# Performance work log

Hardware: AMD Instinct MI355X
Metric: run time of the kernel (lower is better)

## Reference

```python
import jax, jax.numpy as jnp
import numpy as np

K = 8
B = 3.0
DIM = 32
HID = 32
BATCH = 65536
MIN_BW = 1e-3
MIN_BH = 1e-3
MIN_D = 1e-3


def setup_inputs() -> dict:
    key = jax.random.key(0)
    ks = jax.random.split(key, 8)
    L = DIM - 1
    x = jax.random.normal(ks[0], (BATCH, DIM), jnp.float32)
    init_param = jax.random.uniform(ks[1], (3 * K - 1,), jnp.float32, -0.5, 0.5)
    # stacked per-dim FCNN weights; layer l conditions on x[:, :l+1] -> causal zero-mask
    w1 = jax.random.normal(ks[2], (L, L, HID), jnp.float32) * 0.2
    mask = (jnp.arange(L)[None, :] <= jnp.arange(L)[:, None]).astype(jnp.float32)
    w1 = w1 * mask[:, :, None]
    b1 = jax.random.normal(ks[3], (L, HID), jnp.float32) * 0.1
    w2 = jax.random.normal(ks[4], (L, HID, HID), jnp.float32) * 0.2
    b2 = jax.random.normal(ks[5], (L, HID), jnp.float32) * 0.1
    w3 = jax.random.normal(ks[6], (L, HID, 3 * K - 1), jnp.float32) * 0.2
    b3 = jax.random.normal(ks[7], (L, 3 * K - 1), jnp.float32) * 0.1
    return {"x": x, "init_param": init_param, "w1": w1, "b1": b1,
            "w2": w2, "b2": b2, "w3": w3, "b3": b3}


def _rqs_forward(x, Wu, Hu, Du):
    # x: [dim, batch]; Wu, Hu: [dim, batch, K]; Du: [dim, batch, K-1]
    inside = (x >= -B) & (x <= B)
    xc = jnp.clip(x, -B, B)
    # bin widths
    widths = jax.nn.softmax(Wu, axis=-1)
    widths = MIN_BW + (1.0 - MIN_BW * K) * widths
    cw = jnp.cumsum(widths, axis=-1)
    cw = jnp.concatenate([jnp.zeros(cw.shape[:-1] + (1,), cw.dtype), cw], axis=-1)
    cw = 2.0 * B * cw - B
    cw = cw.at[..., 0].set(-B).at[..., -1].set(B)
    widths = cw[..., 1:] - cw[..., :-1]
    # bin heights
    heights = jax.nn.softmax(Hu, axis=-1)
    heights = MIN_BH + (1.0 - MIN_BH * K) * heights
    ch = jnp.cumsum(heights, axis=-1)
    ch = jnp.concatenate([jnp.zeros(ch.shape[:-1] + (1,), ch.dtype), ch], axis=-1)
    ch = 2.0 * B * ch - B
    ch = ch.at[..., 0].set(-B).at[..., -1].set(B)
    heights = ch[..., 1:] - ch[..., :-1]
    # knot derivatives, edges pinned so softplus(const)+min_d = 1
    const = float(np.log(np.exp(1.0 - MIN_D) - 1.0))
    pad = jnp.full(Du.shape[:-1] + (1,), const, Du.dtype)
    derivs = MIN_D + jax.nn.softplus(jnp.concatenate([pad, Du, pad], axis=-1))  # [.., K+1]
    # bin search (searchsorted on cumwidths, eps bump on last edge)
    cw_s = cw.at[..., -1].add(1e-6)
    idx = jnp.sum((xc[..., None] >= cw_s).astype(jnp.int32), axis=-1) - 1
    idx = jnp.clip(idx, 0, K - 1)
    g = lambda a: jnp.take_along_axis(a, idx[..., None], axis=-1)[..., 0]
    in_cw = g(cw)
    in_w = g(widths)
    in_ch = g(ch)
    in_h = g(heights)
    in_delta = g(heights / widths)
    d0 = g(derivs)
    d1 = g(derivs[..., 1:])
    theta = (xc - in_cw) / in_w
    tt = theta * (1.0 - theta)
    num = in_h * (in_delta * theta ** 2 + d0 * tt)
    den = in_delta + (d0 + d1 - 2.0 * in_delta) * tt
    out = in_ch + num / den
    dnum = in_delta ** 2 * (d1 * theta ** 2 + 2.0 * in_delta * tt + d0 * (1.0 - theta) ** 2)
    ld = jnp.log(dnum) - 2.0 * jnp.log(den)
    out = jnp.where(inside, out, x)  # identity tails
    ld = jnp.where(inside, ld, 0.0)
    return out, ld


def reference(x, init_param, w1, b1, w2, b2, w3, b3):
    # all per-dim conditioners at once (w1 is causally masked in setup)
    h1 = jnp.tanh(jnp.einsum('bd,ldh->lbh', x[:, :DIM - 1], w1) + b1[:, None, :])
    h2 = jnp.tanh(jnp.einsum('lbh,lhg->lbg', h1, w2) + b2[:, None, :])
    out = jnp.einsum('lbh,lho->lbo', h2, w3) + b3[:, None, :]  # [dim-1, batch, 3K-1]
    p0 = jnp.broadcast_to(init_param, (1, x.shape[0], 3 * K - 1))
    params = jnp.concatenate([p0, out], axis=0)  # [dim, batch, 3K-1]
    Wu = 2.0 * B * jax.nn.softmax(params[..., :K], axis=-1)
    Hu = 2.0 * B * jax.nn.softmax(params[..., K:2 * K], axis=-1)
    Du = jax.nn.softplus(params[..., 2 * K:])
    z_t, ld = _rqs_forward(x.T, Wu, Hu, Du)  # [dim, batch]
    return z_t.T, jnp.sum(ld, axis=0)
```

## Files before the change

kernel.cpp:

```cpp
#include <hip/hip_runtime.h>
#include <hip/hip_bf16.h>
#include <cmath>

constexpr int KN   = 8;
constexpr int NPAR = 23;
constexpr int DD   = 32;
constexpr float BND   = 3.0f;
constexpr float MINBW = 1e-3f;
constexpr float MIND  = 1e-3f;

#define TPB   256
#define ROWS  256
#define GDIMS 4
#define WST   40
#define PSTH  28
#define RECB  8192

#define LGKM_FENCE() asm volatile("s_waitcnt lgkmcnt(0)" ::: "memory")

typedef __attribute__((ext_vector_type(8))) short short8;
typedef __attribute__((ext_vector_type(4))) float float4v;
typedef __attribute__((ext_vector_type(2))) __fp16 fp16x2;

#define RCP(x) __builtin_amdgcn_rcpf(x)

__device__ __forceinline__ short f2bf(float f) {
    unsigned u = __float_as_uint(f);
    u += 0x7fffu + ((u >> 16) & 1u);
    return (short)(u >> 16);
}

__device__ __forceinline__ int pkbf(float a, float b) {
    union { __hip_bfloat162 v; int i; } u;
    u.v = __float22bfloat162_rn(make_float2(a, b));
    return u.i;
}

__device__ __forceinline__ int pkh(float a, float b) {
    union { fp16x2 h; int i; } u;
    u.h = __builtin_amdgcn_cvt_pkrtz(a, b);
    return u.i;
}

__device__ __forceinline__ float fast_tanh(float x) {
    float e = __expf(2.0f * x);
    return 1.0f - 2.0f * RCP(e + 1.0f);
}

__device__ __forceinline__ float softplus_fast(float v) {
    return __logf(1.0f + __expf(v));
}

__device__ __forceinline__ float rqs_apply(float xv, const float* p, float& ldout) {
    float cw[KN + 1], ch[KN + 1];
    {
        float t0[KN]; float s = 0.f;
#pragma unroll
        for (int k = 0; k < KN; ++k) { t0[k] = __expf(p[k]); s += t0[k]; }
        float inv = (2.0f * BND) * RCP(s);
        float e2[KN]; float s2 = 0.f;
#pragma unroll
        for (int k = 0; k < KN; ++k) { e2[k] = __expf(inv * t0[k]); s2 += e2[k]; }
        float fac = (1.0f - MINBW * KN) * RCP(s2);
        float c = 0.f;
        cw[0] = -BND;
#pragma unroll
        for (int k = 0; k < KN; ++k) { c += MINBW + fac * e2[k]; cw[k + 1] = 2.0f * BND * c - BND; }
        cw[KN] = BND;
    }
    {
        float t0[KN]; float s = 0.f;
#pragma unroll
        for (int k = 0; k < KN; ++k) { t0[k] = __expf(p[KN + k]); s += t0[k]; }
        float inv = (2.0f * BND) * RCP(s);
        float e2[KN]; float s2 = 0.f;
#pragma unroll
        for (int k = 0; k < KN; ++k) { e2[k] = __expf(inv * t0[k]); s2 += e2[k]; }
        float fac = (1.0f - MINBW * KN) * RCP(s2);
        float c = 0.f;
        ch[0] = -BND;
#pragma unroll
        for (int k = 0; k < KN; ++k) { c += MINBW + fac * e2[k]; ch[k + 1] = 2.0f * BND * c - BND; }
        ch[KN] = BND;
    }

    float xc = fminf(fmaxf(xv, -BND), BND);
    float in_cw = cw[0], in_w = cw[1] - cw[0];
    float in_ch = ch[0], in_h = ch[1] - ch[0];
    float dl0 = 0.0f, dl1 = p[2 * KN];
    bool e0 = true, e1 = false;
#pragma unroll
    for (int k = 1; k < KN; ++k) {
        bool c = (xc >= cw[k]);
        in_cw = c ? cw[k]            : in_cw;
        in_w  = c ? (cw[k+1]-cw[k])  : in_w;
        in_ch = c ? ch[k]            : in_ch;
        in_h  = c ? (ch[k+1]-ch[k])  : in_h;
        dl0   = c ? p[2*KN + k - 1]  : dl0;
        if (k < KN - 1) dl1 = c ? p[2*KN + k] : dl1;
        if (k == 1)      e0 = !c;
        if (k == KN - 1) e1 = c;
    }
    float d0 = e0 ? 1.0f : (MIND + softplus_fast(softplus_fast(dl0)));
    float d1 = e1 ? 1.0f : (MIND + softplus_fast(softplus_fast(dl1)));

    float rw    = RCP(in_w);
    float th    = (xc - in_cw) * rw;
    float delta = in_h * rw;
    float tt    = th * (1.0f - th);
    float th2   = th * th;
    float num   = in_h * (delta * th2 + d0 * tt);
    float den   = delta + (d0 + d1 - 2.0f * delta) * tt;
    float z     = in_ch + num * RCP(den);
    float omt   = 1.0f - th;
    float dnum  = delta * delta * (d1 * th2 + 2.0f * delta * tt + d0 * omt * omt);
    float ldv   = __logf(dnum) - 2.0f * __logf(den);

    bool inside = (xv >= -BND) && (xv <= BND);
    ldout = inside ? ldv : 0.0f;
    return inside ? z : xv;
}

__device__ __forceinline__ short8 xpose_h(float4v cA, float4v cB,
                                          int odd, int sl_a, int sl_b, bool qlow) {
    int a0 = pkbf(fast_tanh(cA[0]), fast_tanh(cA[1]));
    int a1 = pkbf(fast_tanh(cA[2]), fast_tanh(cA[3]));
    int b0 = pkbf(fast_tanh(cB[0]), fast_tanh(cB[1]));
    int b1 = pkbf(fast_tanh(cB[2]), fast_tanh(cB[3]));
    int p0 = odd ? b0 : a0, p1 = odd ? b1 : a1;
    int p2 = odd ? a0 : b0, p3 = odd ? a1 : b1;
    int g0 = __shfl(p0, sl_a, 64);
    int g1 = __shfl(p1, sl_a, 64);
    int g2 = __shfl(p2, sl_b, 64);
    int g3 = __shfl(p3, sl_b, 64);
    union { int4 i; short8 s; } u;
    u.i = qlow ? make_int4(g0, g1, g2, g3) : make_int4(g2, g3, g0, g1);
    return u.s;
}

__device__ __forceinline__ float4v f4v(float4 v) {
    float4v r; r[0] = v.x; r[1] = v.y; r[2] = v.z; r[3] = v.w; return r;
}

struct WFrag {
    short8 w1a, w1b, w2a, w2b, w3a, w3b;
    float4v bA1, bB1, bA2, bB2, bA3, bB3;
};

__device__ __forceinline__ WFrag load_wfrag(const char* __restrict__ wbuf,
                                            int l, int ln, int q) {
    const char* rec = wbuf + (size_t)l * RECB;
    const short* rw = (const short*)rec;
    const float* rb = (const float*)(rec + 7680);
    WFrag f;
    f.w1a = *(const short8*)&rw[ln * WST + q * 8];
    f.w1b = *(const short8*)&rw[(16 + ln) * WST + q * 8];
    f.w2a = *(const short8*)&rw[1280 + ln * WST + q * 8];
    f.w2b = *(const short8*)&rw[1280 + (16 + ln) * WST + q * 8];
    f.w3a = *(const short8*)&rw[2560 + ln * WST + q * 8];
    f.w3b = *(const short8*)&rw[2560 + (16 + ln) * WST + q * 8];
    f.bA1 = f4v(*(const float4*)&rb[4 * q]);
    f.bB1 = f4v(*(const float4*)&rb[16 + 4 * q]);
    f.bA2 = f4v(*(const float4*)&rb[32 + 4 * q]);
    f.bB2 = f4v(*(const float4*)&rb[48 + 4 * q]);
    f.bA3 = f4v(*(const float4*)&rb[64 + 4 * q]);
    f.bB3 = f4v(*(const float4*)&rb[80 + 4 * q]);
    return f;
}

extern "C" __global__ void __launch_bounds__(256)
k_prep(const float* __restrict__ w1, const float* __restrict__ b1,
       const float* __restrict__ w2, const float* __restrict__ b2,
       const float* __restrict__ w3, const float* __restrict__ b3,
       char* __restrict__ wbuf, float* __restrict__ ldo, int B)
{
    const int l = blockIdx.x, tid = threadIdx.x;
    if (l >= 31) {
        const int zb = l - 31;
        const int chunk = B >> 6;
        float4* dst = (float4*)(ldo + (size_t)zb * chunk);
        for (int i = tid; i < (chunk >> 2); i += 256)
            dst[i] = make_float4(0.f, 0.f, 0.f, 0.f);
        return;
    }
    short* r1 = (short*)(wbuf + (size_t)l * RECB);
    short* r2 = r1 + 1280;
    short* r3 = r2 + 1280;
    float* f1 = (float*)(wbuf + (size_t)l * RECB + 7680);
    float* f2 = f1 + 32;
    float* f3 = f2 + 32;
    const float* g1 = w1 + (size_t)l * 992;
    const float* g2 = w2 + (size_t)l * 1024;
    const float* g3 = w3 + (size_t)l * 736;
    for (int i = tid; i < 1280; i += 256) {
        int n = i / WST, k = i - WST * n;
        r1[i] = (k < 31) ? f2bf(g1[k * 32 + n]) : (short)0;
        r2[i] = (k < 32) ? f2bf(g2[k * 32 + n]) : (short)0;
        r3[i] = (n < 23 && k < 32) ? f2bf(g3[k * 23 + n]) : (short)0;
    }
    if (tid < 32) { f1[tid] = b1[(size_t)l * 32 + tid]; f2[tid] = b2[(size_t)l * 32 + tid]; }
    if (tid < 32) f3[tid] = (tid < 23) ? b3[(size_t)l * 23 + tid] : 0.0f;
}

extern "C" __global__ void __launch_bounds__(TPB, 2)
k_nsf(const float* __restrict__ x,
      const float* __restrict__ p0,
      const char* __restrict__ wbuf,
      float* __restrict__ zo, float* __restrict__ ldo, int B)
{
    __shared__ __align__(16) _Float16 sPa[ROWS * PSTH];
    __shared__ __align__(16) _Float16 sPb[ROWS * PSTH];

    const int tid  = threadIdx.x;
    const int lane = tid & 63;
    const int wv   = tid >> 6;
    const int q    = lane >> 4;
    const int ln   = lane & 15;
    const int qb   = q & 1;
    const bool qlow = (q < 2);
    const int s_even = ln + 32 * qb;
    const int s_odd  = s_even + 16;
    const int sl_a = qlow ? s_even : s_odd;
    const int sl_b = qlow ? s_odd  : s_even;
    const int g    = blockIdx.y;
    const int ly0  = GDIMS * g;
    const long long rowbase = (long long)blockIdx.x * ROWS;
    const long long row = rowbase + tid;

    float xarr[GDIMS];
    {
        float4 xs = *(const float4*)(x + row * DD + ly0);
        xarr[0] = xs.x; xarr[1] = xs.y; xarr[2] = xs.z; xarr[3] = xs.w;
    }

    short8 au[4];
#pragma unroll
    for (int t = 0; t < 4; ++t) {
        const int m0 = 64 * wv + 16 * t;
        const float4* xp = (const float4*)(x + (rowbase + m0 + ln) * DD + q * 8);
        float4 uu = xp[0], vv = xp[1];
        union { int4 i; short8 s; } c;
        c.i = make_int4(pkbf(uu.x, uu.y), pkbf(uu.z, uu.w),
                        pkbf(vv.x, vv.y), pkbf(vv.z, vv.w));
        au[t] = c.s;
    }

    float zreg[GDIMS];
    float ldacc = 0.0f;

    auto gemm_pack = [&](const WFrag& wf, _Float16* buf) {
        float4v cA[4], cB[4];
#pragma unroll
        for (int t = 0; t < 4; ++t) {
            cA[t] = __builtin_amdgcn_mfma_f32_16x16x32_bf16(wf.w1a, au[t], wf.bA1, 0, 0, 0);
            cB[t] = __builtin_amdgcn_mfma_f32_16x16x32_bf16(wf.w1b, au[t], wf.bB1, 0, 0, 0);
        }
        short8 hf[4];
#pragma unroll
        for (int t = 0; t < 4; ++t)
            hf[t] = xpose_h(cA[t], cB[t], qb, sl_a, sl_b, qlow);
#pragma unroll
        for (int t = 0; t < 4; ++t) {
            cA[t] = __builtin_amdgcn_mfma_f32_16x16x32_bf16(wf.w2a, hf[t], wf.bA2, 0, 0, 0);
            cB[t] = __builtin_amdgcn_mfma_f32_16x16x32_bf16(wf.w2b, hf[t], wf.bB2, 0, 0, 0);
        }
#pragma unroll
        for (int t = 0; t < 4; ++t)
            hf[t] = xpose_h(cA[t], cB[t], qb, sl_a, sl_b, qlow);
#pragma unroll
        for (int t = 0; t < 4; ++t) {
            cA[t] = __builtin_amdgcn_mfma_f32_16x16x32_bf16(wf.w3a, hf[t], wf.bA3, 0, 0, 0);
            cB[t] = __builtin_amdgcn_mfma_f32_16x16x32_bf16(wf.w3b, hf[t], wf.bB3, 0, 0, 0);
        }
#pragma unroll
        for (int t = 0; t < 4; ++t) {
            const int m0 = 64 * wv + 16 * t;
            int2* prow = (int2*)&buf[(m0 + ln) * PSTH];
            prow[q] = make_int2(pkh(cA[t][0], cA[t][1]), pkh(cA[t][2], cA[t][3]));
            if (qlow)
                prow[4 + q] = make_int2(pkh(cB[t][0], cB[t][1]), pkh(cB[t][2], cB[t][3]));
        }
    };

    auto do_spline = [&](const _Float16* buf, int j) {
        const int2* pp = (const int2*)&buf[tid * PSTH];
        float pr[24];
#pragma unroll
        for (int u = 0; u < 6; ++u) {
            union { int2 i; _Float16 h[4]; } hv;
            hv.i = pp[u];
            pr[4*u+0] = (float)hv.h[0];
            pr[4*u+1] = (float)hv.h[1];
            pr[4*u+2] = (float)hv.h[2];
            pr[4*u+3] = (float)hv.h[3];
        }
        float ld;
        zreg[j] = rqs_apply(xarr[j], pr, ld);
        ldacc += ld;
    };

    const int jg = (ly0 == 0) ? 1 : 0;
    WFrag wf = load_wfrag(wbuf, ly0 + jg - 1, ln, q);

#pragma unroll
    for (int jj = 0; jj < GDIMS; ++jj) {
        if (jj < jg) continue;
        _Float16* buf = (jj & 1) ? sPb : sPa;
        if (jj > jg) LGKM_FENCE();
        gemm_pack(wf, buf);
        if (jj + 1 < GDIMS) wf = load_wfrag(wbuf, ly0 + jj, ln, q);
        if (jj == jg) {
            if (ly0 == 0) {
                float pr[NPAR];
#pragma unroll
                for (int k = 0; k < NPAR; ++k) pr[k] = p0[k];
                float ld;
                zreg[0] = rqs_apply(xarr[0], pr, ld);
                ldacc += ld;
            }
        } else {
            do_spline(((jj - 1) & 1) ? sPb : sPa, jj - 1);
        }
    }
    LGKM_FENCE();
    do_spline(((GDIMS - 1) & 1) ? sPb : sPa, GDIMS - 1);

    float4 zv = make_float4(zreg[0], zreg[1], zreg[2], zreg[3]);
    *(float4*)(zo + row * DD + ly0) = zv;
    unsafeAtomicAdd(&ldo[row], ldacc);
}

extern "C" void kernel_launch(void* const* d_in, const int* in_sizes, int n_in,
                              void* d_out, int out_size, void* d_ws, size_t ws_size,
                              hipStream_t stream) {
    const float* x  = (const float*)d_in[0];
    const float* p0 = (const float*)d_in[1];
    const float* w1 = (const float*)d_in[2];
    const float* b1 = (const float*)d_in[3];
    const float* w2 = (const float*)d_in[4];
    const float* b2 = (const float*)d_in[5];
    const float* w3 = (const float*)d_in[6];
    const float* b3 = (const float*)d_in[7];

    const int B = in_sizes[0] / DD;
    float* zo  = (float*)d_out;
    float* ldo = zo + (size_t)B * DD;
    char* wbuf = (char*)d_ws;

    hipLaunchKernelGGL(k_prep, dim3(95), dim3(256), 0, stream,
                       w1, b1, w2, b2, w3, b3, wbuf, ldo, B);
    hipLaunchKernelGGL(k_nsf, dim3(B / ROWS, DD / GDIMS), dim3(TPB), 0, stream,
                       x, p0, wbuf, zo, ldo, B);
}
```

Baseline: 143.5 us.

## Process spline dims in pairs to interleave independent transcendental chains

Restructures the per-thread loop over four output dims into two phases. Each phase computes two conditioner GEMMs back to back, then evaluates both rational-quadratic splines together with interleaved loops. The aim is more instruction-level parallelism across the exp/log/rcp chains in place of the previous software pipeline that overlapped one GEMM with the prior dim's spline. The cost is higher register pressure and the loss of GEMM/spline overlap.

```diff
diff --git a/kernel.cpp b/kernel.cpp
--- a/kernel.cpp
+++ b/kernel.cpp
@@ -51,74 +51,90 @@
     return __logf(1.0f + __expf(v));
 }
 
-__device__ __forceinline__ float rqs_apply(float xv, const float* p, float& ldout) {
-    float cw[KN + 1], ch[KN + 1];
+__device__ __forceinline__ void rqs_apply2(const float xv[2],
+                                           const float* __restrict__ prA,
+                                           const float* __restrict__ prB,
+                                           float z[2], float& ldacc) {
+    const float* q4[4] = { prA, prA + KN, prB, prB + KN };
+    float kn[4][KN + 1];
     {
-        float t0[KN]; float s = 0.f;
-#pragma unroll
-        for (int k = 0; k < KN; ++k) { t0[k] = __expf(p[k]); s += t0[k]; }
-        float inv = (2.0f * BND) * RCP(s);
-        float e2[KN]; float s2 = 0.f;
-#pragma unroll
-        for (int k = 0; k < KN; ++k) { e2[k] = __expf(inv * t0[k]); s2 += e2[k]; }
-        float fac = (1.0f - MINBW * KN) * RCP(s2);
-        float c = 0.f;
-        cw[0] = -BND;
-#pragma unroll
-        for (int k = 0; k < KN; ++k) { c += MINBW + fac * e2[k]; cw[k + 1] = 2.0f * BND * c - BND; }
-        cw[KN] = BND;
-    }
-    {
-        float t0[KN]; float s = 0.f;
-#pragma unroll
-        for (int k = 0; k < KN; ++k) { t0[k] = __expf(p[KN + k]); s += t0[k]; }
-        float inv = (2.0f * BND) * RCP(s);
-        float e2[KN]; float s2 = 0.f;
-#pragma unroll
-        for (int k = 0; k < KN; ++k) { e2[k] = __expf(inv * t0[k]); s2 += e2[k]; }
-        float fac = (1.0f - MINBW * KN) * RCP(s2);
-        float c = 0.f;
-        ch[0] = -BND;
-#pragma unroll
-        for (int k = 0; k < KN; ++k) { c += MINBW + fac * e2[k]; ch[k + 1] = 2.0f * BND * c - BND; }
-        ch[KN] = BND;
-    }
-
-    float xc = fminf(fmaxf(xv, -BND), BND);
-    float in_cw = cw[0], in_w = cw[1] - cw[0];
-    float in_ch = ch[0], in_h = ch[1] - ch[0];
-    float dl0 = 0.0f, dl1 = p[2 * KN];
-    bool e0 = true, e1 = false;
-#pragma unroll
-    for (int k = 1; k < KN; ++k) {
-        bool c = (xc >= cw[k]);
-        in_cw = c ? cw[k]            : in_cw;
-        in_w  = c ? (cw[k+1]-cw[k])  : in_w;
-        in_ch = c ? ch[k]            : in_ch;
-        in_h  = c ? (ch[k+1]-ch[k])  : in_h;
-        dl0   = c ? p[2*KN + k - 1]  : dl0;
-        if (k < KN - 1) dl1 = c ? p[2*KN + k] : dl1;
-        if (k == 1)      e0 = !c;
-        if (k == KN - 1) e1 = c;
-    }
-    float d0 = e0 ? 1.0f : (MIND + softplus_fast(softplus_fast(dl0)));
-    float d1 = e1 ? 1.0f : (MIND + softplus_fast(softplus_fast(dl1)));
-
-    float rw    = RCP(in_w);
-    float th    = (xc - in_cw) * rw;
-    float delta = in_h * rw;
-    float tt    = th * (1.0f - th);
-    float th2   = th * th;
-    float num   = in_h * (delta * th2 + d0 * tt);
-    float den   = delta + (d0 + d1 - 2.0f * delta) * tt;
-    float z     = in_ch + num * RCP(den);
-    float omt   = 1.0f - th;
-    float dnum  = delta * delta * (d1 * th2 + 2.0f * delta * tt + d0 * omt * omt);
-    float ldv   = __logf(dnum) - 2.0f * __logf(den);
-
-    bool inside = (xv >= -BND) && (xv <= BND);
-    ldout = inside ? ldv : 0.0f;
-    return inside ? z : xv;
+        float t0[4][KN], s[4] = {0.f, 0.f, 0.f, 0.f};
+#pragma unroll
+        for (int k = 0; k < KN; ++k)
+#pragma unroll
+            for (int i = 0; i < 4; ++i) { t0[i][k] = __expf(q4[i][k]); s[i] += t0[i][k]; }
+        float inv[4];
+#pragma unroll
+        for (int i = 0; i < 4; ++i) inv[i] = (2.0f * BND) * RCP(s[i]);
+        float e2[4][KN], s2[4] = {0.f, 0.f, 0.f, 0.f};
+#pragma unroll
+        for (int k = 0; k < KN; ++k)
+#pragma unroll
+            for (int i = 0; i < 4; ++i) { e2[i][k] = __expf(inv[i] * t0[i][k]); s2[i] += e2[i][k]; }
+        float fac[4], c[4] = {0.f, 0.f, 0.f, 0.f};
+#pragma unroll
+        for (int i = 0; i < 4; ++i) { fac[i] = (1.0f - MINBW * KN) * RCP(s2[i]); kn[i][0] = -BND; }
+#pragma unroll
+        for (int k = 0; k < KN; ++k)
+#pragma unroll
+            for (int i = 0; i < 4; ++i) {
+                c[i] += MINBW + fac[i] * e2[i][k];
+                kn[i][k + 1] = 2.0f * BND * c[i] - BND;
+            }
+#pragma unroll
+        for (int i = 0; i < 4; ++i) kn[i][KN] = BND;
+    }
+
+    const float* P2[2] = { prA, prB };
+    float xc[2], in_cw[2], in_w[2], in_ch[2], in_h[2], dl0[2], dl1[2];
+    bool e0[2], e1[2];
+#pragma unroll
+    for (int i = 0; i < 2; ++i) {
+        xc[i]    = fminf(fmaxf(xv[i], -BND), BND);
+        in_cw[i] = kn[2*i][0];   in_w[i] = kn[2*i][1]   - kn[2*i][0];
+        in_ch[i] = kn[2*i+1][0]; in_h[i] = kn[2*i+1][1] - kn[2*i+1][0];
+        dl0[i] = 0.0f; dl1[i] = P2[i][2 * KN];
+        e0[i] = true;  e1[i] = false;
+    }
+#pragma unroll
+    for (int k = 1; k < KN; ++k)
+#pragma unroll
+        for (int i = 0; i < 2; ++i) {
+            bool c = (xc[i] >= kn[2*i][k]);
+            in_cw[i] = c ? kn[2*i][k]               : in_cw[i];
+            in_w[i]  = c ? (kn[2*i][k+1]-kn[2*i][k]) : in_w[i];
+            in_ch[i] = c ? kn[2*i+1][k]             : in_ch[i];
+            in_h[i]  = c ? (kn[2*i+1][k+1]-kn[2*i+1][k]) : in_h[i];
+            dl0[i]   = c ? P2[i][2*KN + k - 1]      : dl0[i];
+            if (k < KN - 1) dl1[i] = c ? P2[i][2*KN + k] : dl1[i];
+            if (k == 1)      e0[i] = !c;
+            if (k == KN - 1) e1[i] = c;
+        }
+
+    float d0[2], d1[2];
+#pragma unroll
+    for (int i = 0; i < 2; ++i) {
+        d0[i] = e0[i] ? 1.0f : (MIND + softplus_fast(softplus_fast(dl0[i])));
+        d1[i] = e1[i] ? 1.0f : (MIND + softplus_fast(softplus_fast(dl1[i])));
+    }
+
+#pragma unroll
+    for (int i = 0; i < 2; ++i) {
+        float rw    = RCP(in_w[i]);
+        float th    = (xc[i] - in_cw[i]) * rw;
+        float delta = in_h[i] * rw;
+        float tt    = th * (1.0f - th);
+        float th2   = th * th;
+        float num   = in_h[i] * (delta * th2 + d0[i] * tt);
+        float den   = delta + (d0[i] + d1[i] - 2.0f * delta) * tt;
+        float zz    = in_ch[i] + num * RCP(den);
+        float omt   = 1.0f - th;
+        float dnum  = delta * delta * (d1[i] * th2 + 2.0f * delta * tt + d0[i] * omt * omt);
+        float ldv   = __logf(dnum) - 2.0f * __logf(den);
+        bool inside = (xv[i] >= -BND) && (xv[i] <= BND);
+        z[i] = inside ? zz : xv[i];
+        ldacc += inside ? ldv : 0.0f;
+    }
 }
 
 __device__ __forceinline__ short8 xpose_h(float4v cA, float4v cB,
@@ -282,9 +298,8 @@
         }
     };
 
-    auto do_spline = [&](const _Float16* buf, int j) {
+    auto load_pr = [&](const _Float16* buf, float* pr) {
         const int2* pp = (const int2*)&buf[tid * PSTH];
-        float pr[24];
 #pragma unroll
         for (int u = 0; u < 6; ++u) {
             union { int2 i; _Float16 h[4]; } hv;
@@ -294,36 +309,42 @@
             pr[4*u+2] = (float)hv.h[2];
             pr[4*u+3] = (float)hv.h[3];
         }
-        float ld;
-        zreg[j] = rqs_apply(xarr[j], pr, ld);
-        ldacc += ld;
     };
 
-    const int jg = (ly0 == 0) ? 1 : 0;
-    WFrag wf = load_wfrag(wbuf, ly0 + jg - 1, ln, q);
-
-#pragma unroll
-    for (int jj = 0; jj < GDIMS; ++jj) {
-        if (jj < jg) continue;
-        _Float16* buf = (jj & 1) ? sPb : sPa;
-        if (jj > jg) LGKM_FENCE();
-        gemm_pack(wf, buf);
-        if (jj + 1 < GDIMS) wf = load_wfrag(wbuf, ly0 + jj, ln, q);
-        if (jj == jg) {
-            if (ly0 == 0) {
-                float pr[NPAR];
-#pragma unroll
-                for (int k = 0; k < NPAR; ++k) pr[k] = p0[k];
-                float ld;
-                zreg[0] = rqs_apply(xarr[0], pr, ld);
-                ldacc += ld;
-            }
+    {
+        float prA[24], prB[24];
+        if (ly0 == 0) {
+            gemm_pack(load_wfrag(wbuf, 0, ln, q), sPb);
+            LGKM_FENCE();
+#pragma unroll
+            for (int k = 0; k < NPAR; ++k) prA[k] = p0[k];
+            prA[23] = 0.0f;
+            load_pr(sPb, prB);
         } else {
-            do_spline(((jj - 1) & 1) ? sPb : sPa, jj - 1);
-        }
+            gemm_pack(load_wfrag(wbuf, ly0 - 1, ln, q), sPa);
+            gemm_pack(load_wfrag(wbuf, ly0,     ln, q), sPb);
+            LGKM_FENCE();
+            load_pr(sPa, prA);
+            load_pr(sPb, prB);
+        }
+        float xv2[2] = { xarr[0], xarr[1] };
+        float zz[2];
+        rqs_apply2(xv2, prA, prB, zz, ldacc);
+        zreg[0] = zz[0]; zreg[1] = zz[1];
     }
     LGKM_FENCE();
-    do_spline(((GDIMS - 1) & 1) ? sPb : sPa, GDIMS - 1);
+    {
+        gemm_pack(load_wfrag(wbuf, ly0 + 1, ln, q), sPa);
+        gemm_pack(load_wfrag(wbuf, ly0 + 2, ln, q), sPb);
+        LGKM_FENCE();
+        float prA[24], prB[24];
+        load_pr(sPa, prA);
+        load_pr(sPb, prB);
+        float xv2[2] = { xarr[2], xarr[3] };
+        float zz[2];
+        rqs_apply2(xv2, prA, prB, zz, ldacc);
+        zreg[2] = zz[0]; zreg[3] = zz[1];
+    }
 
     float4 zv = make_float4(zreg[0], zreg[1], zreg[2], zreg[3]);
     *(float4*)(zo + row * DD + ly0) = zv;
```

New measurement: 144.6 us. About the same (+0.7%).
